# Kernel optimization log

Hardware: AMD Instinct MI355X
Metric: run time of the kernel (lower is better)

Reference implementation:

```python
import jax, jax.numpy as jnp
import numpy as np

SWIGLU_LIMIT = 7.0
NUM_EXPERTS = 8
HIDDEN = 2880
INTER = 2880
TOKENS = 512
TOP_K = 4
W_SCALE = 0.02  # realistic init scale; keeps activations off the clamp rails


def setup_inputs() -> dict:
    key = jax.random.key(0)
    k_t, k_idx, k_gu, k_gub, k_d, k_db = jax.random.split(key, 6)
    t = jax.random.normal(k_t, (TOKENS, HIDDEN), dtype=jnp.float32)
    expert_indices = jax.random.randint(k_idx, (TOKENS, TOP_K), 0, NUM_EXPERTS)
    gate_up_proj = jax.random.normal(k_gu, (NUM_EXPERTS, 2 * INTER, HIDDEN), dtype=jnp.float32) * W_SCALE
    gate_up_proj_bias = jax.random.normal(k_gub, (NUM_EXPERTS, 2 * INTER), dtype=jnp.float32) * W_SCALE
    down_proj = jax.random.normal(k_d, (NUM_EXPERTS, HIDDEN, INTER), dtype=jnp.float32) * W_SCALE
    down_proj_bias = jax.random.normal(k_db, (NUM_EXPERTS, HIDDEN), dtype=jnp.float32) * W_SCALE
    return {
        "t": t,
        "expert_indices": expert_indices,
        "gate_up_proj": gate_up_proj,
        "gate_up_proj_bias": gate_up_proj_bias,
        "down_proj": down_proj,
        "down_proj_bias": down_proj_bias,
    }


def reference(t, expert_indices, gate_up_proj, gate_up_proj_bias, down_proj, down_proj_bias):
    # Same math as torch's gate_up_proj[expert_indices] einsum, but we avoid
    # materializing [B,K,2I,H] duplicated weights: compute all experts then gather.
    # h_all: [B, E, 2I]
    h_all = jnp.einsum('eck,bk->bec', gate_up_proj, t)
    # gather per (token, selected expert): [B, K, 2I]
    h = jnp.take_along_axis(h_all, expert_indices[:, :, None], axis=1)
    h = h + gate_up_proj_bias[expert_indices]
    x_glu = jnp.minimum(h[..., ::2], SWIGLU_LIMIT)
    x_lin = jnp.clip(h[..., 1::2], -SWIGLU_LIMIT, SWIGLU_LIMIT)
    out_glu = x_glu * jax.nn.sigmoid(1.702 * x_glu)
    u = out_glu * (x_lin + 1.0)  # [B, K, I]
    # down-proj for all experts then gather: y_all [B, K, E, H]
    y_all = jnp.einsum('ehi,bki->bkeh', down_proj, u)
    y = jnp.take_along_axis(y_all, expert_indices[:, :, None, None], axis=2)[:, :, 0, :]
    y = y + down_proj_bias[expert_indices]
    return y  # [B, K, H]
```

## Files before the change

### kernel.cpp

```cpp
#include <hip/hip_runtime.h>
#include <hip/hip_bf16.h>

#define HIDDEN   2880
#define INTER    2880
#define NEXP     8
#define GUP_ROWS 5760
#define NPAIR    2048

#define BM    320
#define PLANE_B 5120
#define KT64_B  40960
#define NKT64   45
#define KT32_B  20480
#define NKT32   90

#define MAXTILES 15
#define IMG_BYTES ((size_t)MAXTILES * NKT64 * KT64_B)

using bf16x8 = __attribute__((ext_vector_type(8))) short;
using f32x4  = __attribute__((ext_vector_type(4))) float;

typedef const __attribute__((address_space(1))) unsigned GBuf;
typedef __attribute__((address_space(3))) unsigned LBuf;

__device__ __forceinline__ void gl2lds(const void* g, void* l) {
  __builtin_amdgcn_global_load_lds((GBuf*)g, (LBuf*)l, 16, 0, 0);
}
#define WAITVM(N) { asm volatile("s_waitcnt vmcnt(" #N ")" ::: "memory"); \
                    __builtin_amdgcn_sched_barrier(0); }
__device__ __forceinline__ void barrier() {
  __builtin_amdgcn_sched_barrier(0);
  __builtin_amdgcn_s_barrier();
  __builtin_amdgcn_sched_barrier(0);
}

__device__ __forceinline__ unsigned cvt2bf(float a, float b) {
  union { __hip_bfloat16 h; unsigned short s; } x, y;
  x.h = __float2bfloat16(a);
  y.h = __float2bfloat16(b);
  return (unsigned)x.s | ((unsigned)y.s << 16);
}
__device__ __forceinline__ bf16x8 cvt8(const float4& lo, const float4& hi) {
  union { bf16x8 v; unsigned u[4]; } r;
  r.u[0] = cvt2bf(lo.x, lo.y);
  r.u[1] = cvt2bf(lo.z, lo.w);
  r.u[2] = cvt2bf(hi.x, hi.y);
  r.u[3] = cvt2bf(hi.z, hi.w);
  return r.v;
}

__global__ void route_count(const int* __restrict__ eidx, int* __restrict__ meta) {
  __shared__ int cnt[NEXP];
  int t = threadIdx.x;
  if (t < NEXP) cnt[t] = 0;
  __syncthreads();
  for (int a = t; a < NPAIR; a += 256) atomicAdd(&cnt[eidx[a]], 1);
  __syncthreads();
  if (t == 0) {
    int off = 0, toff = 0;
    for (int e = 0; e < NEXP; ++e) {
      meta[e] = cnt[e];
      meta[8 + e] = off;
      meta[16 + e] = off;
      meta[24 + e] = toff;
      off += cnt[e];
      toff += (cnt[e] + BM - 1) / BM;
    }
  }
}

__global__ void route_scatter(const int* __restrict__ eidx, int* __restrict__ meta,
                              int* __restrict__ list) {
  int a = blockIdx.x * 256 + threadIdx.x;
  int e = eidx[a];
  int pos = atomicAdd(&meta[16 + e], 1);
  list[pos] = a;
}

__global__ void gather_a(const float* __restrict__ t, const int* __restrict__ eidx,
                         const int* __restrict__ meta, const int* __restrict__ list,
                         char* __restrict__ atile) {
  const int i = blockIdx.x;
  const int a = list[i];
  const int e = eidx[a];
  const int r = i - meta[8 + e];
  const int tile = meta[24 + e] + r / BM;
  const int row = r % BM;
  const float* src = t + (size_t)(a >> 2) * HIDDEN;
  for (int ch = threadIdx.x; ch < HIDDEN / 8; ch += 256) {
    const float4* s = (const float4*)(src + ch * 8);
    float4 v0 = s[0], v1 = s[1];
    uint4 w;
    w.x = cvt2bf(v0.x, v0.y); w.y = cvt2bf(v0.z, v0.w);
    w.z = cvt2bf(v1.x, v1.y); w.w = cvt2bf(v1.z, v1.w);
    *(uint4*)(atile + ((size_t)tile * 360 + ch) * PLANE_B + row * 16) = w;
  }
}

__global__ __launch_bounds__(256, 2)
void gemm1_swiglu(const char* __restrict__ aimg,
                  const float* __restrict__ gup,
                  const float* __restrict__ gub,
                  const int* __restrict__ meta,
                  char* __restrict__ uimg)
{
  const int e = blockIdx.x, nt = blockIdx.y, mt = blockIdx.z;
  const int n_e = meta[e];
  const int m0 = mt * BM;
  if (m0 >= n_e) return;
  const int tile = meta[24 + e] + mt;
  int rows = n_e - m0; if (rows > BM) rows = BM;
  int V = (rows + 63) >> 6; if (V < 4) V = 4;

  __shared__ __align__(16) char lds[2 * 32768];

  const int tid = threadIdx.x, lane = tid & 63, wid = tid >> 6;
  const int wm = wid;
  const int kq = lane >> 4, l15 = lane & 15;

  const char* aSrc = aimg + (size_t)tile * 360 * PLANE_B;
  const char* srcA[5]; int dstA[5];
  #pragma unroll
  for (int j = 0; j < 5; ++j) {
    int c = wid * 5 + j;
    srcA[j] = aSrc + c * 1024 + lane * 16;
    dstA[j] = c * 1024;
  }
  const char* srcB[3]; int dstB[3];
  #pragma unroll
  for (int j = 0; j < 3; ++j) {
    int cb = wid * 3 + j;
    int col = nt * 96 + cb * 8 + (lane >> 3);
    int g = (lane & 7) >> 1, h = lane & 1;
    srcB[j] = (const char*)gup + (size_t)(e * GUP_ROWS + col) * (HIDDEN * 4)
              + (((g ^ (col & 3)) << 5) | (h << 4));
    dstB[j] = 20480 + cb * 1024;
  }

  auto STAGE = [&](int kt, int buf) {
    char* dst = lds + buf * 32768;
    #pragma unroll
    for (int j = 0; j < 5; ++j)
      if (j < V)
        gl2lds(srcA[j] + (size_t)kt * KT32_B, dst + dstA[j]);
    #pragma unroll
    for (int j = 0; j < 3; ++j)
      gl2lds(srcB[j] + (size_t)kt * 128, dst + dstB[j]);
  };

  f32x4 acc[5][6];
  #pragma unroll
  for (int fm = 0; fm < 5; ++fm)
    #pragma unroll
    for (int fn = 0; fn < 6; ++fn)
      acc[fm][fn] = f32x4{0.f, 0.f, 0.f, 0.f};

  auto COMP = [&](int buf) {
    const char* base = lds + buf * 32768;
    const char* aB = base + kq * PLANE_B + (wm * 80 + l15) * 16;
    bf16x8 af[5], bf[6];
    #pragma unroll
    for (int fm = 0; fm < 5; ++fm) af[fm] = *(const bf16x8*)(aB + fm * 256);
    #pragma unroll
    for (int fn = 0; fn < 6; ++fn) {
      int col = fn * 16 + l15;
      const char* cp = base + 20480 + col * 128 + ((kq ^ (col & 3)) << 5);
      float4 lo = *(const float4*)cp;
      float4 hi = *(const float4*)(cp + 16);
      bf[fn] = cvt8(lo, hi);
    }
    #pragma unroll
    for (int fm = 0; fm < 5; ++fm)
      #pragma unroll
      for (int fn = 0; fn < 6; ++fn)
        acc[fm][fn] = __builtin_amdgcn_mfma_f32_16x16x32_bf16(af[fm], bf[fn], acc[fm][fn], 0, 0, 0);
  };


  STAGE(0, 0);
  for (int kt = 0; kt < NKT32; ++kt) {
    if (kt + 1 < NKT32) {
      STAGE(kt + 1, (kt + 1) & 1);
      if (V == 5) { WAITVM(8) } else { WAITVM(7) }
    } else { WAITVM(0) }
    barrier();
    COMP(kt & 1);
    barrier();
  }

  #pragma unroll
  for (int fm = 0; fm < 5; ++fm) {
    #pragma unroll
    for (int fn = 0; fn < 6; ++fn) {
      const int colg = nt * 96 + fn * 16 + l15;
      const float bias = gub[e * GUP_ROWS + colg];
      #pragma unroll
      for (int j = 0; j < 4; ++j) {
        float h = acc[fm][fn][j] + bias;
        float other = __shfl_xor(h, 1, 64);
        int rowin = wm * 80 + fm * 16 + kq * 4 + j;
        if (!(lane & 1) && rowin < rows) {
          float xg = fminf(h, 7.0f);
          float xl = fminf(fmaxf(other, -7.0f), 7.0f);
          float og = xg / (1.0f + __expf(-1.702f * xg));
          float uv = og * (xl + 1.0f);
          int uc = colg >> 1;
          *(__hip_bfloat16*)(uimg + ((size_t)tile * 360 + (uc >> 3)) * PLANE_B +
              rowin * 16 + (uc & 7) * 2) = __float2bfloat16(uv);
        }
      }
    }
  }
}

__global__ __launch_bounds__(512, 1)
void gemm2_down(const char* __restrict__ uimg,
                const float* __restrict__ dwn,
                const float* __restrict__ dbias,
                const int* __restrict__ meta,
                const int* __restrict__ list,
                float* __restrict__ out)
{
  constexpr int BN_ = 96;
  constexpr int BBUF = BN_ * 256;

  const int e = blockIdx.x, nt = blockIdx.y, mt = blockIdx.z;
  const int n_e = meta[e];
  const int m0 = mt * BM;
  if (m0 >= n_e) return;
  const int tile = meta[24 + e] + mt;
  int rows = n_e - m0; if (rows > BM) rows = BM;
  int V = (rows + 63) >> 6; if (V < 4) V = 4;

  __shared__ __align__(16) char lds[2 * KT64_B + 2 * BBUF];
  char* ldsB = lds + 2 * KT64_B;

  const int tid = threadIdx.x, lane = tid & 63, wid = tid >> 6;
  const int wm = wid >> 1, wn = wid & 1;
  const int kq = lane >> 4, l15 = lane & 15;

  const char* aSrcBase = uimg + (size_t)tile * 360 * PLANE_B;
  const char* srcA[5]; int dstA[5];
  #pragma unroll
  for (int j = 0; j < 5; ++j) {
    srcA[j] = aSrcBase + wid * PLANE_B + j * 1024 + lane * 16;
    dstA[j] = wid * PLANE_B + j * 1024;
  }
  const char* srcB[3]; int dstB[3];
  #pragma unroll
  for (int j = 0; j < 3; ++j) {
    int cb = wid * 3 + j;
    int col = nt * BN_ + cb * 4 + (lane >> 4);
    int s16 = lane & 15;
    int swz = (((s16 >> 1) ^ (col & 7)) << 5) | ((s16 & 1) << 4);
    srcB[j] = (const char*)dwn + ((size_t)(e * HIDDEN + col) * INTER) * 4 + swz;
    dstB[j] = cb * 1024;
  }

  auto STAGE = [&](int kt, int buf) {
    #pragma unroll
    for (int j = 0; j < 5; ++j)
      if (j < V)
        gl2lds(srcA[j] + (size_t)kt * KT64_B, lds + buf * KT64_B + dstA[j]);
    #pragma unroll
    for (int j = 0; j < 3; ++j)
      gl2lds(srcB[j] + (size_t)kt * 256, ldsB + buf * BBUF + dstB[j]);
  };

  f32x4 acc[5][3];
  #pragma unroll
  for (int fm = 0; fm < 5; ++fm)
    #pragma unroll
    for (int fn = 0; fn < 3; ++fn)
      acc[fm][fn] = f32x4{0.f, 0.f, 0.f, 0.f};

  auto COMP = [&](int buf) {
    const char* aT = lds + buf * KT64_B;
    const char* bT = ldsB + buf * BBUF;
    #pragma unroll
    for (int s = 0; s < 2; ++s) {
      const char* aB = aT + (s * 4 + kq) * PLANE_B + (wm * 80 + l15) * 16;
      bf16x8 af[5], bf[3];
      #pragma unroll
      for (int fm = 0; fm < 5; ++fm) af[fm] = *(const bf16x8*)(aB + fm * 256);
      #pragma unroll
      for (int fn = 0; fn < 3; ++fn) {
        int col = wn * 48 + fn * 16 + l15;
        int slot = ((s * 4 + kq) ^ (col & 7)) << 5;
        const char* cp = bT + col * 256 + slot;
        float4 lo = *(const float4*)cp;
        float4 hi = *(const float4*)(cp + 16);
        bf[fn] = cvt8(lo, hi);
      }
      #pragma unroll
      for (int fm = 0; fm < 5; ++fm)
        #pragma unroll
        for (int fn = 0; fn < 3; ++fn)
          acc[fm][fn] = __builtin_amdgcn_mfma_f32_16x16x32_bf16(af[fm], bf[fn], acc[fm][fn], 0, 0, 0);
    }
  };

  STAGE(0, 0);
  for (int kt = 0; kt < NKT64; ++kt) {
    if (kt + 1 < NKT64) {
      STAGE(kt + 1, (kt + 1) & 1);
      if (V == 5) { WAITVM(8) } else { WAITVM(7) }
    } else { WAITVM(0) }
    barrier();
    COMP(kt & 1);
    barrier();
  }

  const int base = meta[8 + e];
  #pragma unroll
  for (int fm = 0; fm < 5; ++fm) {
    #pragma unroll
    for (int j = 0; j < 4; ++j) {
      int rin = wm * 80 + fm * 16 + kq * 4 + j;
      int aidx = (rin < rows) ? list[base + m0 + rin] : -1;
      #pragma unroll
      for (int fn = 0; fn < 3; ++fn) {
        int col = nt * BN_ + wn * 48 + fn * 16 + l15;
        if (aidx >= 0)
          out[(size_t)aidx * HIDDEN + col] = acc[fm][fn][j] + dbias[e * HIDDEN + col];
      }
    }
  }
}

extern "C" void kernel_launch(void* const* d_in, const int* in_sizes, int n_in,
                              void* d_out, int out_size, void* d_ws, size_t ws_size,
                              hipStream_t stream) {
  const float* t     = (const float*)d_in[0];
  const int*   eidx  = (const int*)d_in[1];
  const float* gup   = (const float*)d_in[2];
  const float* gub   = (const float*)d_in[3];
  const float* dwn   = (const float*)d_in[4];
  const float* dbias = (const float*)d_in[5];
  float* out = (float*)d_out;

  char* ws = (char*)d_ws;
  char* atile = ws;
  char* utile = ws + IMG_BYTES;
  int* meta = (int*)(ws + 2 * IMG_BYTES);
  int* list = meta + 32;

  route_count<<<1, 256, 0, stream>>>(eidx, meta);
  route_scatter<<<NPAIR / 256, 256, 0, stream>>>(eidx, meta, list);
  gather_a<<<NPAIR, 256, 0, stream>>>(t, eidx, meta, list, atile);

  dim3 g1(NEXP, GUP_ROWS / 96, 2);
  gemm1_swiglu<<<g1, 256, 0, stream>>>(atile, gup, gub, meta, utile);

  dim3 g2(NEXP, HIDDEN / 96, 2);
  gemm2_down<<<g2, 512, 0, stream>>>(utile, dwn, dbias, meta, list, out);
}
```

Before: 300.1 us.

## Convert gemm1 weights to bf16 via registers before LDS, shrink N tile for occupancy

gemm1 now loads its fp32 weight tile into registers a step ahead, converts it to bf16 once, and writes the packed bf16 into a smaller LDS buffer. Before, the fp32 was staged straight into LDS and reconverted in every compute pass. The N tile drops from 96 to 64 columns, which cuts LDS to 48KB and the accumulators to 5x4, and launch bounds rise to 3 blocks per CU. The costs are more blocks, so the A tile is reloaded more often, plus an lgkmcnt wait and an extra register-staged load in the loop.

```diff
diff --git a/kernel.cpp b/kernel.cpp
--- a/kernel.cpp
+++ b/kernel.cpp
@@ -28,6 +28,8 @@
 }
 #define WAITVM(N) { asm volatile("s_waitcnt vmcnt(" #N ")" ::: "memory"); \
                     __builtin_amdgcn_sched_barrier(0); }
+#define WAITLGKM0 { asm volatile("s_waitcnt lgkmcnt(0)" ::: "memory"); \
+                    __builtin_amdgcn_sched_barrier(0); }
 __device__ __forceinline__ void barrier() {
   __builtin_amdgcn_sched_barrier(0);
   __builtin_amdgcn_s_barrier();
@@ -39,14 +41,6 @@
   x.h = __float2bfloat16(a);
   y.h = __float2bfloat16(b);
   return (unsigned)x.s | ((unsigned)y.s << 16);
-}
-__device__ __forceinline__ bf16x8 cvt8(const float4& lo, const float4& hi) {
-  union { bf16x8 v; unsigned u[4]; } r;
-  r.u[0] = cvt2bf(lo.x, lo.y);
-  r.u[1] = cvt2bf(lo.z, lo.w);
-  r.u[2] = cvt2bf(hi.x, hi.y);
-  r.u[3] = cvt2bf(hi.z, hi.w);
-  return r.v;
 }
 
 __global__ void route_count(const int* __restrict__ eidx, int* __restrict__ meta) {
@@ -97,7 +91,8 @@
   }
 }
 
-__global__ __launch_bounds__(256, 2)
+#define B1BASE 40960
+__global__ __launch_bounds__(256, 3)
 void gemm1_swiglu(const char* __restrict__ aimg,
                   const float* __restrict__ gup,
                   const float* __restrict__ gub,
@@ -112,7 +107,7 @@
   int rows = n_e - m0; if (rows > BM) rows = BM;
   int V = (rows + 63) >> 6; if (V < 4) V = 4;
 
-  __shared__ __align__(16) char lds[2 * 32768];
+  __shared__ __align__(16) char lds[49152];
 
   const int tid = threadIdx.x, lane = tid & 63, wid = tid >> 6;
   const int wm = wid;
@@ -126,73 +121,72 @@
     srcA[j] = aSrc + c * 1024 + lane * 16;
     dstA[j] = c * 1024;
   }
-  const char* srcB[3]; int dstB[3];
-  #pragma unroll
-  for (int j = 0; j < 3; ++j) {
-    int cb = wid * 3 + j;
-    int col = nt * 96 + cb * 8 + (lane >> 3);
-    int g = (lane & 7) >> 1, h = lane & 1;
-    srcB[j] = (const char*)gup + (size_t)(e * GUP_ROWS + col) * (HIDDEN * 4)
-              + (((g ^ (col & 3)) << 5) | (h << 4));
-    dstB[j] = 20480 + cb * 1024;
-  }
-
-  auto STAGE = [&](int kt, int buf) {
-    char* dst = lds + buf * 32768;
+  const int bcol = tid >> 2, bseg = tid & 3;
+  const float* bSrc = gup + (size_t)(e * GUP_ROWS + nt * 64 + bcol) * HIDDEN + bseg * 8;
+  const int bDst = bseg * 1024 + bcol * 16;
+
+  float4 rb0, rb1;
+  auto LOADB = [&](int kt) {
+    rb0 = *(const float4*)(bSrc + (size_t)kt * 32);
+    rb1 = *(const float4*)(bSrc + (size_t)kt * 32 + 4);
+  };
+  auto STAGEA = [&](int kt, int buf) {
+    char* dst = lds + buf * 20480;
     #pragma unroll
     for (int j = 0; j < 5; ++j)
       if (j < V)
         gl2lds(srcA[j] + (size_t)kt * KT32_B, dst + dstA[j]);
-    #pragma unroll
-    for (int j = 0; j < 3; ++j)
-      gl2lds(srcB[j] + (size_t)kt * 128, dst + dstB[j]);
-  };
-
-  f32x4 acc[5][6];
+  };
+  auto WRITEB = [&](int buf) {
+    uint4 w;
+    w.x = cvt2bf(rb0.x, rb0.y); w.y = cvt2bf(rb0.z, rb0.w);
+    w.z = cvt2bf(rb1.x, rb1.y); w.w = cvt2bf(rb1.z, rb1.w);
+    *(uint4*)(lds + B1BASE + buf * 4096 + bDst) = w;
+    WAITLGKM0
+  };
+
+  f32x4 acc[5][4];
   #pragma unroll
   for (int fm = 0; fm < 5; ++fm)
     #pragma unroll
-    for (int fn = 0; fn < 6; ++fn)
+    for (int fn = 0; fn < 4; ++fn)
       acc[fm][fn] = f32x4{0.f, 0.f, 0.f, 0.f};
 
   auto COMP = [&](int buf) {
-    const char* base = lds + buf * 32768;
-    const char* aB = base + kq * PLANE_B + (wm * 80 + l15) * 16;
-    bf16x8 af[5], bf[6];
+    const char* aB = lds + buf * 20480 + kq * PLANE_B + (wm * 80 + l15) * 16;
+    const char* bB = lds + B1BASE + buf * 4096 + kq * 1024;
+    bf16x8 af[5], bf[4];
     #pragma unroll
     for (int fm = 0; fm < 5; ++fm) af[fm] = *(const bf16x8*)(aB + fm * 256);
     #pragma unroll
-    for (int fn = 0; fn < 6; ++fn) {
-      int col = fn * 16 + l15;
-      const char* cp = base + 20480 + col * 128 + ((kq ^ (col & 3)) << 5);
-      float4 lo = *(const float4*)cp;
-      float4 hi = *(const float4*)(cp + 16);
-      bf[fn] = cvt8(lo, hi);
-    }
+    for (int fn = 0; fn < 4; ++fn) bf[fn] = *(const bf16x8*)(bB + (fn * 16 + l15) * 16);
     #pragma unroll
     for (int fm = 0; fm < 5; ++fm)
       #pragma unroll
-      for (int fn = 0; fn < 6; ++fn)
+      for (int fn = 0; fn < 4; ++fn)
         acc[fm][fn] = __builtin_amdgcn_mfma_f32_16x16x32_bf16(af[fm], bf[fn], acc[fm][fn], 0, 0, 0);
   };
 
-
-  STAGE(0, 0);
+  LOADB(0);
+  STAGEA(0, 0);
+  WRITEB(0);
   for (int kt = 0; kt < NKT32; ++kt) {
     if (kt + 1 < NKT32) {
-      STAGE(kt + 1, (kt + 1) & 1);
-      if (V == 5) { WAITVM(8) } else { WAITVM(7) }
+      LOADB(kt + 1);
+      STAGEA(kt + 1, (kt + 1) & 1);
+      if (V == 5) { WAITVM(7) } else { WAITVM(6) }
     } else { WAITVM(0) }
     barrier();
     COMP(kt & 1);
+    if (kt + 1 < NKT32) WRITEB((kt + 1) & 1);
     barrier();
   }
 
   #pragma unroll
   for (int fm = 0; fm < 5; ++fm) {
     #pragma unroll
-    for (int fn = 0; fn < 6; ++fn) {
-      const int colg = nt * 96 + fn * 16 + l15;
+    for (int fn = 0; fn < 4; ++fn) {
+      const int colg = nt * 64 + fn * 16 + l15;
       const float bias = gub[e * GUP_ROWS + colg];
       #pragma unroll
       for (int j = 0; j < 4; ++j) {
@@ -290,7 +284,10 @@
         const char* cp = bT + col * 256 + slot;
         float4 lo = *(const float4*)cp;
         float4 hi = *(const float4*)(cp + 16);
-        bf[fn] = cvt8(lo, hi);
+        union { bf16x8 v; unsigned u[4]; } r;
+        r.u[0] = cvt2bf(lo.x, lo.y); r.u[1] = cvt2bf(lo.z, lo.w);
+        r.u[2] = cvt2bf(hi.x, hi.y); r.u[3] = cvt2bf(hi.z, hi.w);
+        bf[fn] = r.v;
       }
       #pragma unroll
       for (int fm = 0; fm < 5; ++fm)
@@ -349,7 +346,7 @@
   route_scatter<<<NPAIR / 256, 256, 0, stream>>>(eidx, meta, list);
   gather_a<<<NPAIR, 256, 0, stream>>>(t, eidx, meta, list, atile);
 
-  dim3 g1(NEXP, GUP_ROWS / 96, 2);
+  dim3 g1(NEXP, GUP_ROWS / 64, 2);
   gemm1_swiglu<<<g1, 256, 0, stream>>>(atile, gup, gub, meta, utile);
 
   dim3 g2(NEXP, HIDDEN / 96, 2);
```

Result: slower. 327.0 us (+9.0%).
